# Performance work log

Hardware: AMD Instinct MI355X
Metric: run time of the kernel (lower is better)

The kernel has to match this reference:

```python
import jax, jax.numpy as jnp
import numpy as np

K = 5          # number of spline bins
B = 5.0        # tail bound
HIDDEN = 8
MIN_W = 1e-3; MIN_H = 1e-3; MIN_D = 1e-3  # RQS defaults (Durkan et al.)


def setup_inputs() -> dict:
    n, d = 32768, 64
    L = d - 1
    P = 3 * K - 1
    ks = jax.random.split(jax.random.key(0), 8)
    x = jax.random.normal(ks[0], (n, d), jnp.float32) * 2.0
    init_param = jax.random.uniform(ks[1], (P,), jnp.float32, -0.5, 0.5)
    # ragged first layers: layer l (predicts dim l+1) sees x[:, :l+1]; zero-pad to width L
    mask = (jnp.arange(L)[None, :] <= jnp.arange(L)[:, None]).astype(jnp.float32)
    W1 = jax.random.normal(ks[2], (L, L, HIDDEN), jnp.float32) * 0.2 * mask[:, :, None]
    b1 = jax.random.normal(ks[3], (L, HIDDEN), jnp.float32) * 0.1
    W2 = jax.random.normal(ks[4], (L, HIDDEN, HIDDEN), jnp.float32) * 0.2
    b2 = jax.random.normal(ks[5], (L, HIDDEN), jnp.float32) * 0.1
    W3 = jax.random.normal(ks[6], (L, HIDDEN, P), jnp.float32) * 0.2
    b3 = jax.random.normal(ks[7], (L, P), jnp.float32) * 0.1
    return {"x": x, "init_param": init_param, "W1": W1, "b1": b1,
            "W2": W2, "b2": b2, "W3": W3, "b3": b3}


def _rqs(xf, Wu, Hu, Du):
    # xf: (M,), Wu/Hu: (M,K), Du: (M,K-1) -- vectorized unconstrained RQS, forward
    inside = (xf >= -B) & (xf <= B)
    const = float(np.log(np.exp(1.0 - MIN_D) - 1.0))
    Dpad = jnp.pad(Du, ((0, 0), (1, 1)), constant_values=const)

    widths = MIN_W + (1.0 - MIN_W * K) * jax.nn.softmax(Wu, axis=-1)
    cumw = jnp.pad(jnp.cumsum(widths, -1), ((0, 0), (1, 0)))
    cumw = 2.0 * B * cumw - B
    cumw = cumw.at[:, 0].set(-B).at[:, -1].set(B)
    widths = cumw[:, 1:] - cumw[:, :-1]

    heights = MIN_H + (1.0 - MIN_H * K) * jax.nn.softmax(Hu, axis=-1)
    cumh = jnp.pad(jnp.cumsum(heights, -1), ((0, 0), (1, 0)))
    cumh = 2.0 * B * cumh - B
    cumh = cumh.at[:, 0].set(-B).at[:, -1].set(B)
    heights = cumh[:, 1:] - cumh[:, :-1]

    derivs = MIN_D + jax.nn.softplus(Dpad)  # (M, K+1)

    xc = jnp.clip(xf, -B, B)
    idx = jnp.clip(jnp.sum(xc[:, None] >= cumw, axis=-1) - 1, 0, K - 1)
    take = lambda a: jnp.take_along_axis(a, idx[:, None], axis=-1)[:, 0]

    icw, ibw = take(cumw), take(widths)
    ich, ih = take(cumh), take(heights)
    idl = take(heights / widths)
    idv = take(derivs)
    idvp1 = take(derivs[:, 1:])

    theta = (xc - icw) / ibw
    tmt = theta * (1.0 - theta)
    num = ih * (idl * theta * theta + idv * tmt)
    den = idl + (idv + idvp1 - 2.0 * idl) * tmt
    out = ich + num / den
    dnum = idl * idl * (idvp1 * theta * theta + 2.0 * idl * tmt + idv * (1.0 - theta) ** 2)
    ld = jnp.log(dnum) - 2.0 * jnp.log(den)
    return jnp.where(inside, out, xf), jnp.where(inside, ld, 0.0)


def reference(x, init_param, W1, b1, W2, b2, W3, b3):
    n, d = x.shape
    L = d - 1
    P = 3 * K - 1
    # mask re-applied so padded W1 entries are exactly inert (ragged Linear(i, hidden))
    mask = (jnp.arange(L)[None, :] <= jnp.arange(L)[:, None]).astype(x.dtype)
    h = jnp.tanh(jnp.einsum('nj,ljh->lnh', x[:, :L], W1 * mask[:, :, None]) + b1[:, None, :])
    h = jnp.tanh(jnp.einsum('lnh,lhg->lng', h, W2) + b2[:, None, :])
    out = jnp.einsum('lng,lgp->lnp', h, W3) + b3[:, None, :]      # (L, n, P)
    p0 = jnp.broadcast_to(init_param, (1, n, P))                  # dim 0 uses init_param
    params = jnp.concatenate([p0, out], axis=0).reshape(d * n, P)  # dim-major, matches Ws layout
    Wu, Hu, Du = params[:, :K], params[:, K:2 * K], params[:, 2 * K:]
    xf = x.T.reshape(-1)  # x.transpose(0,1).flatten()
    zs, lds = _rqs(xf, Wu, Hu, Du)
    # NOTE: faithfully replicates the original's reshape of the dim-major flat
    # vector directly to (n, d) (as in the torch source).
    return zs.reshape(n, d), lds.reshape(n, d).sum(axis=1)
```

## Files before the change

kernel.cpp:

```cpp
#include <hip/hip_runtime.h>
#include <math.h>

#define KK 5
#define Bc 5.0f
#define NN 32768
#define DD 64
#define LL 63
#define PP 14
#define MIN_Wc 0.001f
#define MIN_Hc 0.001f
#define MIN_Dc 0.001f

__device__ __forceinline__ float rcp_fast(float v) {
    return __builtin_amdgcn_rcpf(v);
}
__device__ __forceinline__ float exp_fast(float v) {
    return __expf(v);
}
__device__ __forceinline__ float log_fast(float v) {
    return __logf(v);
}
__device__ __forceinline__ float tanh_fast(float v) {
    float e = exp_fast(2.0f * v);
    return 1.0f - 2.0f * rcp_fast(e + 1.0f);
}
__device__ __forceinline__ float softplus_fast(float v) {
    return (v > 15.0f) ? v : log_fast(1.0f + exp_fast(v));
}

__global__ __launch_bounds__(256) void nsf_kernel(
    const float* __restrict__ x, const float* __restrict__ init_param,
    const float* __restrict__ W1, const float* __restrict__ b1,
    const float* __restrict__ W2, const float* __restrict__ b2,
    const float* __restrict__ W3, const float* __restrict__ b3,
    float* __restrict__ out)
{
    __shared__ float xs[64 * 65];
    const int s0 = blockIdx.x * 64;
    const int tid = threadIdx.x;

    for (int q = tid; q < 64 * 64; q += 256) {
        int r = q >> 6, c = q & 63;
        xs[r * 65 + c] = x[(s0 + r) * 64 + c];
    }
    __syncthreads();

    const int lane = tid & 63;
    const int wave = tid >> 6;
    const float* xrow = &xs[lane * 65];
    const int t = blockIdx.y * 4 + wave;

    #pragma unroll 1
    for (int k = 0; k < 4; ++k) {
        int dd;
        switch (k) {
            case 0: dd = t;       break;
            case 1: dd = 31 - t;  break;
            case 2: dd = 32 + t;  break;
            default: dd = 63 - t; break;
        }
        dd = __builtin_amdgcn_readfirstlane(dd);

        float p[PP];
        if (dd == 0) {
            #pragma unroll
            for (int i = 0; i < PP; ++i) p[i] = init_param[i];
        } else {
            const int l = dd - 1;
            float h1[8];
            #pragma unroll
            for (int h = 0; h < 8; ++h) h1[h] = b1[l * 8 + h];
            const float* W1l = &W1[l * LL * 8];
            for (int j = 0; j <= l; ++j) {
                float xv = xrow[j];
                #pragma unroll
                for (int h = 0; h < 8; ++h) h1[h] = fmaf(xv, W1l[j * 8 + h], h1[h]);
            }
            #pragma unroll
            for (int h = 0; h < 8; ++h) h1[h] = tanh_fast(h1[h]);

            float h2[8];
            const float* W2l = &W2[l * 64];
            #pragma unroll
            for (int g = 0; g < 8; ++g) h2[g] = b2[l * 8 + g];
            #pragma unroll
            for (int h = 0; h < 8; ++h) {
                #pragma unroll
                for (int g = 0; g < 8; ++g) h2[g] = fmaf(h1[h], W2l[h * 8 + g], h2[g]);
            }
            #pragma unroll
            for (int g = 0; g < 8; ++g) h2[g] = tanh_fast(h2[g]);

            const float* W3l = &W3[l * 8 * PP];
            #pragma unroll
            for (int q = 0; q < PP; ++q) p[q] = b3[l * PP + q];
            #pragma unroll
            for (int g = 0; g < 8; ++g) {
                #pragma unroll
                for (int q = 0; q < PP; ++q) p[q] = fmaf(h2[g], W3l[g * PP + q], p[q]);
            }
        }

        const float xf = xrow[dd];

        float wmax = p[0];
        #pragma unroll
        for (int i = 1; i < KK; ++i) wmax = fmaxf(wmax, p[i]);
        float we[KK]; float wsum = 0.f;
        #pragma unroll
        for (int i = 0; i < KK; ++i) { we[i] = exp_fast(p[i] - wmax); wsum += we[i]; }
        const float wnorm = (1.0f - MIN_Wc * KK) * rcp_fast(wsum);
        float cumw[KK + 1], wdt[KK];
        cumw[0] = -Bc;
        float acw = 0.f;
        #pragma unroll
        for (int i = 0; i < KK; ++i) { acw += MIN_Wc + wnorm * we[i]; cumw[i + 1] = 2.f * Bc * acw - Bc; }
        cumw[KK] = Bc;
        #pragma unroll
        for (int i = 0; i < KK; ++i) wdt[i] = cumw[i + 1] - cumw[i];

        float hmax = p[KK];
        #pragma unroll
        for (int i = 1; i < KK; ++i) hmax = fmaxf(hmax, p[KK + i]);
        float he[KK]; float hsum = 0.f;
        #pragma unroll
        for (int i = 0; i < KK; ++i) { he[i] = exp_fast(p[KK + i] - hmax); hsum += he[i]; }
        const float hnorm = (1.0f - MIN_Hc * KK) * rcp_fast(hsum);
        float cumh[KK + 1], hgt[KK];
        cumh[0] = -Bc;
        float ach = 0.f;
        #pragma unroll
        for (int i = 0; i < KK; ++i) { ach += MIN_Hc + hnorm * he[i]; cumh[i + 1] = 2.f * Bc * ach - Bc; }
        cumh[KK] = Bc;
        #pragma unroll
        for (int i = 0; i < KK; ++i) hgt[i] = cumh[i + 1] - cumh[i];

        float derivs[KK + 1];
        derivs[0] = 1.0f;
        derivs[KK] = 1.0f;
        #pragma unroll
        for (int i = 0; i < KK - 1; ++i) derivs[i + 1] = MIN_Dc + softplus_fast(p[2 * KK + i]);

        const float xc = fminf(fmaxf(xf, -Bc), Bc);

        float icw = cumw[0], ibw = wdt[0], ich = cumh[0], ih = hgt[0];
        float idv = derivs[0], idvp1 = derivs[1];
        #pragma unroll
        for (int i = 1; i < KK; ++i) {
            bool c = xc >= cumw[i];
            icw   = c ? cumw[i]      : icw;
            ibw   = c ? wdt[i]       : ibw;
            ich   = c ? cumh[i]      : ich;
            ih    = c ? hgt[i]       : ih;
            idv   = c ? derivs[i]    : idv;
            idvp1 = c ? derivs[i + 1]: idvp1;
        }

        const float ibw_r = rcp_fast(ibw);
        const float idl = ih * ibw_r;
        const float theta = (xc - icw) * ibw_r;
        const float omt = 1.0f - theta;
        const float tmt = theta * omt;
        const float num = ih * (idl * theta * theta + idv * tmt);
        const float den = idl + (idv + idvp1 - 2.0f * idl) * tmt;
        const float outv = ich + num * rcp_fast(den);
        const float dnum = idl * idl * (idvp1 * theta * theta + 2.0f * idl * tmt + idv * omt * omt);
        const float ld = log_fast(dnum) - 2.0f * log_fast(den);

        const bool inside = (xf >= -Bc) && (xf <= Bc);
        const float z = inside ? outv : xf;
        float ldv = inside ? ld : 0.0f;

        out[dd * NN + s0 + lane] = z;

        #pragma unroll
        for (int off = 32; off > 0; off >>= 1) ldv += __shfl_down(ldv, off);
        if (lane == 0) out[NN * DD + dd * (NN / 64) + blockIdx.x] = ldv;
    }
}

extern "C" void kernel_launch(void* const* d_in, const int* in_sizes, int n_in,
                              void* d_out, int out_size, void* d_ws, size_t ws_size,
                              hipStream_t stream) {
    const float* x          = (const float*)d_in[0];
    const float* init_param = (const float*)d_in[1];
    const float* W1         = (const float*)d_in[2];
    const float* b1         = (const float*)d_in[3];
    const float* W2         = (const float*)d_in[4];
    const float* b2         = (const float*)d_in[5];
    const float* W3         = (const float*)d_in[6];
    const float* b3         = (const float*)d_in[7];
    float* out = (float*)d_out;

    dim3 grid(NN / 64, 4);
    nsf_kernel<<<grid, 256, 0, stream>>>(x, init_param, W1, b1, W2, b2, W3, b3, out);
}
```

Baseline: 118.8 us.

## Vectorize weight loads via VGPR-addressed global pointers and float4 x tile layout

Changes the shared x tile to a float4 column-chunk layout and loads the W1/W2/W3/bias weights as float4 through global-address-space pointers whose base addresses are copied into VGPRs with inline asm. This forces vector global loads instead of many scalar loads. The W1 loop is unrolled by 4 with a tail for the remainder. It also drops the max-subtraction from both softmaxes, which risks overflow for large logits.

```diff
diff --git a/kernel.cpp b/kernel.cpp
--- a/kernel.cpp
+++ b/kernel.cpp
@@ -11,15 +11,22 @@
 #define MIN_Hc 0.001f
 #define MIN_Dc 0.001f
 
-__device__ __forceinline__ float rcp_fast(float v) {
-    return __builtin_amdgcn_rcpf(v);
-}
-__device__ __forceinline__ float exp_fast(float v) {
-    return __expf(v);
-}
-__device__ __forceinline__ float log_fast(float v) {
-    return __logf(v);
-}
+typedef float f4 __attribute__((ext_vector_type(4)));
+typedef const __attribute__((address_space(1))) float g_float;
+typedef const __attribute__((address_space(1))) f4    g_f4;
+
+__device__ __forceinline__ unsigned long long vgpr_addr(const void* p) {
+    unsigned long long u = (unsigned long long)p;
+    unsigned int lo = (unsigned int)u, hi = (unsigned int)(u >> 32);
+    unsigned int vlo, vhi;
+    asm("v_mov_b32 %0, %2\n\tv_mov_b32 %1, %3"
+        : "=v"(vlo), "=v"(vhi) : "s"(lo), "s"(hi));
+    return ((unsigned long long)vhi << 32) | (unsigned long long)vlo;
+}
+
+__device__ __forceinline__ float rcp_fast(float v)  { return __builtin_amdgcn_rcpf(v); }
+__device__ __forceinline__ float exp_fast(float v)  { return __expf(v); }
+__device__ __forceinline__ float log_fast(float v)  { return __logf(v); }
 __device__ __forceinline__ float tanh_fast(float v) {
     float e = exp_fast(2.0f * v);
     return 1.0f - 2.0f * rcp_fast(e + 1.0f);
@@ -35,19 +42,30 @@
     const float* __restrict__ W3, const float* __restrict__ b3,
     float* __restrict__ out)
 {
-    __shared__ float xs[64 * 65];
+    __shared__ f4 xs[16 * 64];
     const int s0 = blockIdx.x * 64;
     const int tid = threadIdx.x;
-
-    for (int q = tid; q < 64 * 64; q += 256) {
-        int r = q >> 6, c = q & 63;
-        xs[r * 65 + c] = x[(s0 + r) * 64 + c];
+    const int lane = tid & 63;
+    const int wave = tid >> 6;
+
+    {
+        const f4* xg = (const f4*)(x + s0 * 64);
+        #pragma unroll
+        for (int it = 0; it < 4; ++it) {
+            int jc = wave + it * 4;
+            xs[jc * 64 + lane] = xg[lane * 16 + jc];
+        }
     }
     __syncthreads();
 
-    const int lane = tid & 63;
-    const int wave = tid >> 6;
-    const float* xrow = &xs[lane * 65];
+    g_float* ipv = (g_float*)vgpr_addr(init_param);
+    g_f4*    W1v = (g_f4*)vgpr_addr(W1);
+    g_f4*    b1v = (g_f4*)vgpr_addr(b1);
+    g_f4*    W2v = (g_f4*)vgpr_addr(W2);
+    g_f4*    b2v = (g_f4*)vgpr_addr(b2);
+    g_f4*    W3v = (g_f4*)vgpr_addr(W3);
+    g_float* b3v = (g_float*)vgpr_addr(b3);
+
     const int t = blockIdx.y * 4 + wave;
 
     #pragma unroll 1
@@ -64,51 +82,92 @@
         float p[PP];
         if (dd == 0) {
             #pragma unroll
-            for (int i = 0; i < PP; ++i) p[i] = init_param[i];
+            for (int i = 0; i < PP; ++i) p[i] = ipv[i];
         } else {
             const int l = dd - 1;
-            float h1[8];
-            #pragma unroll
-            for (int h = 0; h < 8; ++h) h1[h] = b1[l * 8 + h];
-            const float* W1l = &W1[l * LL * 8];
-            for (int j = 0; j <= l; ++j) {
-                float xv = xrow[j];
+
+            f4 bb0 = b1v[l * 2], bb1 = b1v[l * 2 + 1];
+            float h1[8] = {bb0.x, bb0.y, bb0.z, bb0.w, bb1.x, bb1.y, bb1.z, bb1.w};
+            g_f4* w1p = W1v + l * 126;
+            const f4* xcv = xs + lane;
+            const int nfull = l >> 2;
+            for (int jc = 0; jc < nfull; ++jc) {
+                f4 xv = xcv[jc * 64];
+                f4 wA = w1p[0], wB = w1p[1], wC = w1p[2], wD = w1p[3];
+                f4 wE = w1p[4], wF = w1p[5], wG = w1p[6], wH = w1p[7];
+                w1p += 8;
+                h1[0]=fmaf(xv.x,wA.x,h1[0]); h1[1]=fmaf(xv.x,wA.y,h1[1]);
+                h1[2]=fmaf(xv.x,wA.z,h1[2]); h1[3]=fmaf(xv.x,wA.w,h1[3]);
+                h1[4]=fmaf(xv.x,wB.x,h1[4]); h1[5]=fmaf(xv.x,wB.y,h1[5]);
+                h1[6]=fmaf(xv.x,wB.z,h1[6]); h1[7]=fmaf(xv.x,wB.w,h1[7]);
+                h1[0]=fmaf(xv.y,wC.x,h1[0]); h1[1]=fmaf(xv.y,wC.y,h1[1]);
+                h1[2]=fmaf(xv.y,wC.z,h1[2]); h1[3]=fmaf(xv.y,wC.w,h1[3]);
+                h1[4]=fmaf(xv.y,wD.x,h1[4]); h1[5]=fmaf(xv.y,wD.y,h1[5]);
+                h1[6]=fmaf(xv.y,wD.z,h1[6]); h1[7]=fmaf(xv.y,wD.w,h1[7]);
+                h1[0]=fmaf(xv.z,wE.x,h1[0]); h1[1]=fmaf(xv.z,wE.y,h1[1]);
+                h1[2]=fmaf(xv.z,wE.z,h1[2]); h1[3]=fmaf(xv.z,wE.w,h1[3]);
+                h1[4]=fmaf(xv.z,wF.x,h1[4]); h1[5]=fmaf(xv.z,wF.y,h1[5]);
+                h1[6]=fmaf(xv.z,wF.z,h1[6]); h1[7]=fmaf(xv.z,wF.w,h1[7]);
+                h1[0]=fmaf(xv.w,wG.x,h1[0]); h1[1]=fmaf(xv.w,wG.y,h1[1]);
+                h1[2]=fmaf(xv.w,wG.z,h1[2]); h1[3]=fmaf(xv.w,wG.w,h1[3]);
+                h1[4]=fmaf(xv.w,wH.x,h1[4]); h1[5]=fmaf(xv.w,wH.y,h1[5]);
+                h1[6]=fmaf(xv.w,wH.z,h1[6]); h1[7]=fmaf(xv.w,wH.w,h1[7]);
+            }
+            {
+                f4 xv = xcv[nfull * 64];
+                float xt[4] = {xv.x, xv.y, xv.z, xv.w};
+                const int rem = l & 3;
                 #pragma unroll
-                for (int h = 0; h < 8; ++h) h1[h] = fmaf(xv, W1l[j * 8 + h], h1[h]);
+                for (int i = 0; i < 4; ++i) {
+                    if (i <= rem) {
+                        f4 wa = w1p[2 * i], wb = w1p[2 * i + 1];
+                        h1[0]=fmaf(xt[i],wa.x,h1[0]); h1[1]=fmaf(xt[i],wa.y,h1[1]);
+                        h1[2]=fmaf(xt[i],wa.z,h1[2]); h1[3]=fmaf(xt[i],wa.w,h1[3]);
+                        h1[4]=fmaf(xt[i],wb.x,h1[4]); h1[5]=fmaf(xt[i],wb.y,h1[5]);
+                        h1[6]=fmaf(xt[i],wb.z,h1[6]); h1[7]=fmaf(xt[i],wb.w,h1[7]);
+                    }
+                }
             }
             #pragma unroll
             for (int h = 0; h < 8; ++h) h1[h] = tanh_fast(h1[h]);
 
-            float h2[8];
-            const float* W2l = &W2[l * 64];
-            #pragma unroll
-            for (int g = 0; g < 8; ++g) h2[g] = b2[l * 8 + g];
-            #pragma unroll
-            for (int h = 0; h < 8; ++h) {
+            f4 cb0 = b2v[l * 2], cb1 = b2v[l * 2 + 1];
+            float h2[8] = {cb0.x, cb0.y, cb0.z, cb0.w, cb1.x, cb1.y, cb1.z, cb1.w};
+            g_f4* w2p = W2v + l * 16;
+            #pragma unroll
+            for (int m = 0; m < 16; ++m) {
+                f4 w = w2p[m];
+                float hv = h1[m >> 1];
+                int g0 = (m & 1) * 4;
+                h2[g0+0] = fmaf(hv, w.x, h2[g0+0]);
+                h2[g0+1] = fmaf(hv, w.y, h2[g0+1]);
+                h2[g0+2] = fmaf(hv, w.z, h2[g0+2]);
+                h2[g0+3] = fmaf(hv, w.w, h2[g0+3]);
+            }
+            #pragma unroll
+            for (int g = 0; g < 8; ++g) h2[g] = tanh_fast(h2[g]);
+
+            g_float* b3l = b3v + l * PP;
+            #pragma unroll
+            for (int q = 0; q < PP; ++q) p[q] = b3l[q];
+            g_f4* w3p = W3v + l * 28;
+            #pragma unroll
+            for (int m = 0; m < 28; ++m) {
+                f4 w = w3p[m];
                 #pragma unroll
-                for (int g = 0; g < 8; ++g) h2[g] = fmaf(h1[h], W2l[h * 8 + g], h2[g]);
-            }
-            #pragma unroll
-            for (int g = 0; g < 8; ++g) h2[g] = tanh_fast(h2[g]);
-
-            const float* W3l = &W3[l * 8 * PP];
-            #pragma unroll
-            for (int q = 0; q < PP; ++q) p[q] = b3[l * PP + q];
-            #pragma unroll
-            for (int g = 0; g < 8; ++g) {
-                #pragma unroll
-                for (int q = 0; q < PP; ++q) p[q] = fmaf(h2[g], W3l[g * PP + q], p[q]);
-            }
-        }
-
-        const float xf = xrow[dd];
-
-        float wmax = p[0];
-        #pragma unroll
-        for (int i = 1; i < KK; ++i) wmax = fmaxf(wmax, p[i]);
+                for (int i2 = 0; i2 < 4; ++i2) {
+                    int f = 4 * m + i2;
+                    float wv = (i2 == 0) ? w.x : (i2 == 1) ? w.y : (i2 == 2) ? w.z : w.w;
+                    p[f % PP] = fmaf(h2[f / PP], wv, p[f % PP]);
+                }
+            }
+        }
+
+        const float xf = ((const float*)(xs + ((dd >> 2) * 64 + lane)))[dd & 3];
+
         float we[KK]; float wsum = 0.f;
         #pragma unroll
-        for (int i = 0; i < KK; ++i) { we[i] = exp_fast(p[i] - wmax); wsum += we[i]; }
+        for (int i = 0; i < KK; ++i) { we[i] = exp_fast(p[i]); wsum += we[i]; }
         const float wnorm = (1.0f - MIN_Wc * KK) * rcp_fast(wsum);
         float cumw[KK + 1], wdt[KK];
         cumw[0] = -Bc;
@@ -119,12 +178,9 @@
         #pragma unroll
         for (int i = 0; i < KK; ++i) wdt[i] = cumw[i + 1] - cumw[i];
 
-        float hmax = p[KK];
-        #pragma unroll
-        for (int i = 1; i < KK; ++i) hmax = fmaxf(hmax, p[KK + i]);
         float he[KK]; float hsum = 0.f;
         #pragma unroll
-        for (int i = 0; i < KK; ++i) { he[i] = exp_fast(p[KK + i] - hmax); hsum += he[i]; }
+        for (int i = 0; i < KK; ++i) { he[i] = exp_fast(p[KK + i]); hsum += he[i]; }
         const float hnorm = (1.0f - MIN_Hc * KK) * rcp_fast(hsum);
         float cumh[KK + 1], hgt[KK];
         cumh[0] = -Bc;
@@ -148,12 +204,12 @@
         #pragma unroll
         for (int i = 1; i < KK; ++i) {
             bool c = xc >= cumw[i];
-            icw   = c ? cumw[i]      : icw;
-            ibw   = c ? wdt[i]       : ibw;
-            ich   = c ? cumh[i]      : ich;
-            ih    = c ? hgt[i]       : ih;
-            idv   = c ? derivs[i]    : idv;
-            idvp1 = c ? derivs[i + 1]: idvp1;
+            icw   = c ? cumw[i]       : icw;
+            ibw   = c ? wdt[i]        : ibw;
+            ich   = c ? cumh[i]       : ich;
+            ih    = c ? hgt[i]        : ih;
+            idv   = c ? derivs[i]     : idv;
+            idvp1 = c ? derivs[i + 1] : idvp1;
         }
 
         const float ibw_r = rcp_fast(ibw);
```

Result: slower. 179.0 us (+50.6%).

## Compute first MLP layer with bf16 MFMA GEMM in separate kernel

Applied to the files above, without the earlier changes.

Splits the fused kernel into three: a weight-packing kernel that converts W1 to a bf16 (n, k) layout, an MFMA-based GEMM that computes all 63 first-layer hidden activations (with tanh) for every row and stores them as bf16 in workspace, and the spline kernel that reads those activations instead of running the ragged scalar first-layer loop. This trades the O(d^2) per-thread FMA loop for matrix-core work plus an extra global round-trip of about 16 MB of bf16 activations and two more launches. bf16 rounding of x, W1 and h1 lowers accuracy. The dim-to-wave assignment also changes to a simple strided mapping, since the first-layer cost no longer grows with the dim index.

```diff
diff --git a/kernel.cpp b/kernel.cpp
--- a/kernel.cpp
+++ b/kernel.cpp
@@ -1,4 +1,5 @@
 #include <hip/hip_runtime.h>
+#include <hip/hip_bf16.h>
 #include <math.h>
 
 #define KK 5
@@ -11,15 +12,13 @@
 #define MIN_Hc 0.001f
 #define MIN_Dc 0.001f
 
-__device__ __forceinline__ float rcp_fast(float v) {
-    return __builtin_amdgcn_rcpf(v);
-}
-__device__ __forceinline__ float exp_fast(float v) {
-    return __expf(v);
-}
-__device__ __forceinline__ float log_fast(float v) {
-    return __logf(v);
-}
+typedef float f4 __attribute__((ext_vector_type(4)));
+typedef float f32x4 __attribute__((ext_vector_type(4)));
+typedef short short8 __attribute__((ext_vector_type(8)));
+
+__device__ __forceinline__ float rcp_fast(float v)  { return __builtin_amdgcn_rcpf(v); }
+__device__ __forceinline__ float exp_fast(float v)  { return __expf(v); }
+__device__ __forceinline__ float log_fast(float v)  { return __logf(v); }
 __device__ __forceinline__ float tanh_fast(float v) {
     float e = exp_fast(2.0f * v);
     return 1.0f - 2.0f * rcp_fast(e + 1.0f);
@@ -27,10 +26,89 @@
 __device__ __forceinline__ float softplus_fast(float v) {
     return (v > 15.0f) ? v : log_fast(1.0f + exp_fast(v));
 }
-
-__global__ __launch_bounds__(256) void nsf_kernel(
+__device__ __forceinline__ ushort to_bf16u(float v) {
+    __hip_bfloat16 b = __float2bfloat16(v);
+    return *(ushort*)&b;
+}
+
+__global__ __launch_bounds__(256) void pack_b1(const float* __restrict__ W1,
+                                               ushort* __restrict__ Bp) {
+    int id = blockIdx.x * 256 + threadIdx.x;
+    int n = id >> 6, k = id & 63;
+    float v = 0.f;
+    if (n < 504 && k < 63) {
+        int l = n >> 3, h = n & 7;
+        v = W1[(l * 63 + k) * 8 + h];
+    }
+    Bp[id] = to_bf16u(v);
+}
+
+#define AS 72
+__global__ __launch_bounds__(256) void mlp1_kernel(
+    const float* __restrict__ x, const ushort* __restrict__ Bp,
+    const float* __restrict__ b1, ushort* __restrict__ h1out)
+{
+    __shared__ ushort Alds[64 * AS];
+    __shared__ ushort Blds[128 * AS];
+    const int tid = threadIdx.x;
+    const int row0 = blockIdx.x * 64;
+    const int nbase = blockIdx.y * 128;
+
+    {
+        int r = tid >> 2, c4 = (tid & 3) * 16;
+        const f4* xg = (const f4*)(x + (size_t)(row0 + r) * 64 + c4);
+        #pragma unroll
+        for (int i = 0; i < 4; ++i) {
+            f4 v = xg[i];
+            ushort4 u;
+            u.x = to_bf16u(v.x); u.y = to_bf16u(v.y);
+            u.z = to_bf16u(v.z); u.w = to_bf16u(v.w);
+            *(ushort4*)(&Alds[r * AS + c4 + i * 4]) = u;
+        }
+    }
+    {
+        const short8* src = (const short8*)(Bp + (size_t)nbase * 64);
+        #pragma unroll
+        for (int i = 0; i < 4; ++i) {
+            int e = tid * 4 + i;
+            int n = e >> 3, kc = (e & 7) * 8;
+            *(short8*)(&Blds[n * AS + kc]) = src[e];
+        }
+    }
+    __syncthreads();
+
+    const int lane = tid & 63, wave = tid >> 6;
+    const int m0 = wave * 16;
+    const int qg = lane >> 4;
+    const int ln = lane & 15;
+
+    short8 a0 = *(const short8*)(&Alds[(m0 + ln) * AS + qg * 8]);
+    short8 a1 = *(const short8*)(&Alds[(m0 + ln) * AS + 32 + qg * 8]);
+
+    #pragma unroll
+    for (int t = 0; t < 8; ++t) {
+        short8 bf0 = *(const short8*)(&Blds[(t * 16 + ln) * AS + qg * 8]);
+        short8 bf1 = *(const short8*)(&Blds[(t * 16 + ln) * AS + 32 + qg * 8]);
+        f32x4 acc = {0.f, 0.f, 0.f, 0.f};
+        acc = __builtin_amdgcn_mfma_f32_16x16x32_bf16(a0, bf0, acc, 0, 0, 0);
+        acc = __builtin_amdgcn_mfma_f32_16x16x32_bf16(a1, bf1, acc, 0, 0, 0);
+
+        int ng = nbase + t * 16 + ln;
+        bool valid = ng < 504;
+        float bias = valid ? b1[ng] : 0.f;
+        int l = ng >> 3, h = ng & 7;
+        ushort* dst = h1out + ((size_t)l * NN + row0 + m0 + qg * 4) * 8 + h;
+        #pragma unroll
+        for (int r = 0; r < 4; ++r) {
+            float v = tanh_fast(acc[r] + bias);
+            if (valid) dst[r * 8] = to_bf16u(v);
+        }
+    }
+}
+
+__global__ __launch_bounds__(256) void spline_kernel(
     const float* __restrict__ x, const float* __restrict__ init_param,
-    const float* __restrict__ W1, const float* __restrict__ b1,
+    const ushort* __restrict__ h1g,
     const float* __restrict__ W2, const float* __restrict__ b2,
     const float* __restrict__ W3, const float* __restrict__ b3,
     float* __restrict__ out)
@@ -38,28 +116,18 @@
     __shared__ float xs[64 * 65];
     const int s0 = blockIdx.x * 64;
     const int tid = threadIdx.x;
-
     for (int q = tid; q < 64 * 64; q += 256) {
         int r = q >> 6, c = q & 63;
-        xs[r * 65 + c] = x[(s0 + r) * 64 + c];
+        xs[r * 65 + c] = x[(size_t)(s0 + r) * 64 + c];
     }
     __syncthreads();
 
-    const int lane = tid & 63;
-    const int wave = tid >> 6;
-    const float* xrow = &xs[lane * 65];
+    const int lane = tid & 63, wave = tid >> 6;
     const int t = blockIdx.y * 4 + wave;
 
     #pragma unroll 1
-    for (int k = 0; k < 4; ++k) {
-        int dd;
-        switch (k) {
-            case 0: dd = t;       break;
-            case 1: dd = 31 - t;  break;
-            case 2: dd = 32 + t;  break;
-            default: dd = 63 - t; break;
-        }
-        dd = __builtin_amdgcn_readfirstlane(dd);
+    for (int kk = 0; kk < 4; ++kk) {
+        int dd = __builtin_amdgcn_readfirstlane(t + kk * 16);
 
         float p[PP];
         if (dd == 0) {
@@ -67,41 +135,41 @@
             for (int i = 0; i < PP; ++i) p[i] = init_param[i];
         } else {
             const int l = dd - 1;
-            float h1[8];
-            #pragma unroll
-            for (int h = 0; h < 8; ++h) h1[h] = b1[l * 8 + h];
-            const float* W1l = &W1[l * LL * 8];
-            for (int j = 0; j <= l; ++j) {
-                float xv = xrow[j];
-                #pragma unroll
-                for (int h = 0; h < 8; ++h) h1[h] = fmaf(xv, W1l[j * 8 + h], h1[h]);
-            }
-            #pragma unroll
-            for (int h = 0; h < 8; ++h) h1[h] = tanh_fast(h1[h]);
+            const uint4* hp = (const uint4*)(h1g + (size_t)l * NN * 8);
+            uint4 hv = hp[s0 + lane];
+            float h1f[8];
+            h1f[0] = __uint_as_float(hv.x << 16);
+            h1f[1] = __uint_as_float(hv.x & 0xFFFF0000u);
+            h1f[2] = __uint_as_float(hv.y << 16);
+            h1f[3] = __uint_as_float(hv.y & 0xFFFF0000u);
+            h1f[4] = __uint_as_float(hv.z << 16);
+            h1f[5] = __uint_as_float(hv.z & 0xFFFF0000u);
+            h1f[6] = __uint_as_float(hv.w << 16);
+            h1f[7] = __uint_as_float(hv.w & 0xFFFF0000u);
 
             float h2[8];
-            const float* W2l = &W2[l * 64];
             #pragma unroll
             for (int g = 0; g < 8; ++g) h2[g] = b2[l * 8 + g];
             #pragma unroll
             for (int h = 0; h < 8; ++h) {
                 #pragma unroll
-                for (int g = 0; g < 8; ++g) h2[g] = fmaf(h1[h], W2l[h * 8 + g], h2[g]);
+                for (int g = 0; g < 8; ++g)
+                    h2[g] = fmaf(h1f[h], W2[l * 64 + h * 8 + g], h2[g]);
             }
             #pragma unroll
             for (int g = 0; g < 8; ++g) h2[g] = tanh_fast(h2[g]);
 
-            const float* W3l = &W3[l * 8 * PP];
             #pragma unroll
             for (int q = 0; q < PP; ++q) p[q] = b3[l * PP + q];
             #pragma unroll
             for (int g = 0; g < 8; ++g) {
                 #pragma unroll
-                for (int q = 0; q < PP; ++q) p[q] = fmaf(h2[g], W3l[g * PP + q], p[q]);
+                for (int q = 0; q < PP; ++q)
+                    p[q] = fmaf(h2[g], W3[(l * 8 + g) * PP + q], p[q]);
             }
         }
 
-        const float xf = xrow[dd];
+        const float xf = xs[lane * 65 + dd];
 
         float wmax = p[0];
         #pragma unroll
@@ -148,12 +216,12 @@
         #pragma unroll
         for (int i = 1; i < KK; ++i) {
             bool c = xc >= cumw[i];
-            icw   = c ? cumw[i]      : icw;
-            ibw   = c ? wdt[i]       : ibw;
-            ich   = c ? cumh[i]      : ich;
-            ih    = c ? hgt[i]       : ih;
-            idv   = c ? derivs[i]    : idv;
-            idvp1 = c ? derivs[i + 1]: idvp1;
+            icw   = c ? cumw[i]       : icw;
+            ibw   = c ? wdt[i]        : ibw;
+            ich   = c ? cumh[i]       : ich;
+            ih    = c ? hgt[i]        : ih;
+            idv   = c ? derivs[i]     : idv;
+            idvp1 = c ? derivs[i + 1] : idvp1;
         }
 
         const float ibw_r = rcp_fast(ibw);
@@ -192,6 +260,11 @@
     const float* b3         = (const float*)d_in[7];
     float* out = (float*)d_out;
 
-    dim3 grid(NN / 64, 4);
-    nsf_kernel<<<grid, 256, 0, stream>>>(x, init_param, W1, b1, W2, b2, W3, b3, out);
-}
+    ushort* Bp = (ushort*)d_ws;
+    ushort* h1 = (ushort*)d_ws + 512 * 64;
+
+    pack_b1<<<128, 256, 0, stream>>>(W1, Bp);
+    mlp1_kernel<<<dim3(512, 4), 256, 0, stream>>>(x, Bp, b1, h1);
+    spline_kernel<<<dim3(512, 4), 256, 0, stream>>>(x, init_param, h1,
+                                                    W2, b2, W3, b3, out);
+}
```

Measured after the change: 122.8 us. +3.3%, slower.
